# Kernel optimization log

Measured on AMD Instinct MI355X. Metric: run time of the kernel, lower is better.

The kernel has to match this reference:

```python
import jax, jax.numpy as jnp
import numpy as np

VIS_DIM = 4096
HIDDEN_D = 4096
EMB_DIM = 512
B = 128
N_NEG = 2048


def setup_inputs() -> dict:
    key = jax.random.key(0)
    k = jax.random.split(key, 7)
    vfs = jax.random.normal(k[0], (B, VIS_DIM), dtype=jnp.float32)
    p_lfs = jax.random.normal(k[1], (B, EMB_DIM), dtype=jnp.float32)
    n_lfs = jax.random.normal(k[2], (N_NEG, EMB_DIM), dtype=jnp.float32)
    # Linear params (PyTorch layout: W [out, in], y = x @ W.T + b)
    s_h = 1.0 / np.sqrt(VIS_DIM)
    s_e = 1.0 / np.sqrt(HIDDEN_D)
    W_h = jax.random.uniform(k[3], (HIDDEN_D, VIS_DIM), jnp.float32, -s_h, s_h)
    b_h = jax.random.uniform(k[4], (HIDDEN_D,), jnp.float32, -s_h, s_h)
    W_e = jax.random.uniform(k[5], (EMB_DIM, HIDDEN_D), jnp.float32, -s_e, s_e)
    b_e = jax.random.uniform(k[6], (EMB_DIM,), jnp.float32, -s_e, s_e)
    return {"vfs": vfs, "p_lfs": p_lfs, "n_lfs": n_lfs,
            "W_h": W_h, "b_h": b_h, "W_e": W_e, "b_e": b_e}


def _partial_order_sim(hypers, hypos):
    # -||relu(hypers - hypos)||_2 reduced over the last axis
    act = jax.nn.relu(hypers - hypos)
    return -jnp.sqrt(jnp.sum(act * act, axis=-1))


def reference(vfs, p_lfs, n_lfs, W_h, b_h, W_e, b_e):
    # Two plain Linears (NO ReLU in between, matching the original forward)
    vf_hidden = vfs @ W_h.T + b_h            # [B, 4096]
    vf_emb = vf_hidden @ W_e.T + b_e          # [B, emb]
    # positive score per sample
    p_scores = _partial_order_sim(p_lfs, vf_emb)                    # [B]
    # negative scores, batched over all samples at once (replaces per-sample loop)
    n_scores = _partial_order_sim(n_lfs[None, :, :], vf_emb[:, None, :])  # [B, N]
    score_stack = jnp.concatenate([p_scores[:, None], n_scores], axis=1)  # [B, N+1]
    return score_stack
```

## Files before the change

### kernel.cpp

```cpp
#include <hip/hip_runtime.h>

#define B_N  128
#define VIS  4096
#define HID  4096
#define EMB  512
#define NNEG 2048
#define OUTN (NNEG + 1)

using f32x4  = __attribute__((ext_vector_type(4))) float;
using bf16x8 = __attribute__((ext_vector_type(8))) short;

static __device__ __forceinline__ unsigned short f2bf(float f) {
  unsigned u = __builtin_bit_cast(unsigned, f);
  u += 0x7fffu + ((u >> 16) & 1u);
  return (unsigned short)(u >> 16);
}

union U16x8 { unsigned short us[8]; uint4 v; };
union U16x4 { unsigned short us[4]; uint2 v; };

static __device__ __forceinline__ void glds16(const void* g, void* l) {
  __builtin_amdgcn_global_load_lds(
      (const __attribute__((address_space(1))) unsigned*)g,
      (__attribute__((address_space(3))) unsigned*)l, 16, 0, 0);
}

__global__ __launch_bounds__(256) void prep_kernel(
    const float* __restrict__ src, unsigned short* __restrict__ dst,
    float* __restrict__ emb) {
  const int idx = blockIdx.x * 256 + threadIdx.x;
  float4 a = ((const float4*)src)[idx * 2];
  float4 b = ((const float4*)src)[idx * 2 + 1];
  U16x8 pk;
  pk.us[0] = f2bf(a.x); pk.us[1] = f2bf(a.y); pk.us[2] = f2bf(a.z); pk.us[3] = f2bf(a.w);
  pk.us[4] = f2bf(b.x); pk.us[5] = f2bf(b.y); pk.us[6] = f2bf(b.z); pk.us[7] = f2bf(b.w);
  ((uint4*)dst)[idx] = pk.v;
  if (idx < (B_N * EMB / 4))
    ((float4*)emb)[idx] = make_float4(0.f, 0.f, 0.f, 0.f);
}

__global__ __launch_bounds__(512, 2) void gemm1_kernel(
    const unsigned short* __restrict__ Abf, const float* __restrict__ Wh,
    const float* __restrict__ bh, float* __restrict__ Hp) {
  const int n0    = blockIdx.x * 32;
  const int kbase = blockIdx.y * 2048;

  __shared__ __align__(16) unsigned short As[128 * 64];
  __shared__ __align__(16) unsigned short Ws[32 * 64];

  const int t = threadIdx.x, w = t >> 6, lane = t & 63;
  const int m_lane = lane & 15, kq = lane >> 4;
  f32x4 acc[2] = {};

  const int wr = t >> 4, wc = (t & 15) * 4, Gw = (t & 15) >> 1, sub = (t & 1) * 4;
  const float* Wg = Wh + (size_t)(n0 + wr) * VIS + kbase + wc;
  float4 wv = ((const float4*)Wg)[0];
  Wg += 64;

  const int rowA = lane >> 3;
  const int gA   = (lane & 7) ^ rowA;

  for (int kt = 0; kt < 32; ++kt) {
    __syncthreads();
#pragma unroll
    for (int i = 0; i < 2; ++i) {
      const int m = i * 64 + w * 8 + rowA;
      const unsigned short* src = Abf + (size_t)m * VIS + kbase + kt * 64 + gA * 8;
      glds16(src, &As[(i * 512 + w * 64) * 8]);
    }
    {
      U16x4 pk;
      pk.us[0] = f2bf(wv.x); pk.us[1] = f2bf(wv.y); pk.us[2] = f2bf(wv.z); pk.us[3] = f2bf(wv.w);
      *(uint2*)&Ws[wr * 64 + ((Gw ^ (wr & 7)) * 8) + sub] = pk.v;
    }
    if (kt < 31) {
      wv = ((const float4*)Wg)[0];
      Wg += 64;
    }
    __syncthreads();

#pragma unroll
    for (int ks = 0; ks < 2; ++ks) {
      const int Gk = ks * 4 + kq;
      const int m0 = w * 16 + m_lane;
      bf16x8 a0 = *(const bf16x8*)&As[m0 * 64 + ((Gk ^ (m0 & 7)) * 8)];
      const int nA = m_lane, nB = m_lane + 16;
      bf16x8 b0 = *(const bf16x8*)&Ws[nA * 64 + ((Gk ^ (nA & 7)) * 8)];
      bf16x8 b1 = *(const bf16x8*)&Ws[nB * 64 + ((Gk ^ (nB & 7)) * 8)];
      acc[0] = __builtin_amdgcn_mfma_f32_16x16x32_bf16(a0, b0, acc[0], 0, 0, 0);
      acc[1] = __builtin_amdgcn_mfma_f32_16x16x32_bf16(a0, b1, acc[1], 0, 0, 0);
    }
  }

  float* Pd = Hp + (size_t)blockIdx.y * (B_N * HID);
  const int rq = (lane >> 4) * 4;
#pragma unroll
  for (int ni = 0; ni < 2; ++ni) {
    const int ng = n0 + ni * 16 + m_lane;
    const float bias = (blockIdx.y == 0) ? bh[ng] : 0.0f;
#pragma unroll
    for (int r = 0; r < 4; ++r) {
      const int mg = w * 16 + rq + r;
      Pd[(size_t)mg * HID + ng] = acc[ni][r] + bias;
    }
  }
}

__global__ __launch_bounds__(256) void cvt2_kernel(
    const float* __restrict__ Hp, unsigned short* __restrict__ dst) {
  const int idx = blockIdx.x * 256 + threadIdx.x;
  const float* H1 = Hp + (size_t)B_N * HID;
  float4 a0 = ((const float4*)Hp)[idx * 2];
  float4 b0 = ((const float4*)Hp)[idx * 2 + 1];
  float4 a1 = ((const float4*)H1)[idx * 2];
  float4 b1 = ((const float4*)H1)[idx * 2 + 1];
  U16x8 pk;
  pk.us[0] = f2bf(a0.x + a1.x); pk.us[1] = f2bf(a0.y + a1.y);
  pk.us[2] = f2bf(a0.z + a1.z); pk.us[3] = f2bf(a0.w + a1.w);
  pk.us[4] = f2bf(b0.x + b1.x); pk.us[5] = f2bf(b0.y + b1.y);
  pk.us[6] = f2bf(b0.z + b1.z); pk.us[7] = f2bf(b0.w + b1.w);
  ((uint4*)dst)[idx] = pk.v;
}

__global__ __launch_bounds__(256, 2) void gemm2_kernel(
    const unsigned short* __restrict__ Hbf, const float* __restrict__ We,
    const float* __restrict__ be, float* __restrict__ emb) {
  const int n0    = blockIdx.x * 16;
  const int kbase = blockIdx.y * 512;

  __shared__ __align__(16) unsigned short As[128 * 64];
  __shared__ __align__(16) unsigned short Ws[16 * 64];

  const int t = threadIdx.x, w = t >> 6, lane = t & 63;
  const int m_lane = lane & 15, kq = lane >> 4;
  f32x4 acc[2] = {};

  const int wr = t >> 4, wc = (t & 15) * 4;
  const float* Wg = We + (size_t)(n0 + wr) * HID + kbase + wc;
  float4 wv = ((const float4*)Wg)[0];
  Wg += 64;

  const int rowA = lane >> 3;
  const int gA   = (lane & 7) ^ rowA;

  for (int kt = 0; kt < 8; ++kt) {
    __syncthreads();
#pragma unroll
    for (int i = 0; i < 4; ++i) {
      const int m = i * 32 + w * 8 + rowA;
      const unsigned short* src = Hbf + (size_t)m * HID + kbase + kt * 64 + gA * 8;
      glds16(src, &As[(i * 256 + w * 64) * 8]);
    }
    {
      U16x4 pk;
      pk.us[0] = f2bf(wv.x); pk.us[1] = f2bf(wv.y); pk.us[2] = f2bf(wv.z); pk.us[3] = f2bf(wv.w);
      const int G = (t & 15) >> 1;
      *(uint2*)&Ws[wr * 64 + ((G ^ (wr & 7)) * 8) + (t & 1) * 4] = pk.v;
    }
    if (kt < 7) { wv = ((const float4*)Wg)[0]; Wg += 64; }
    __syncthreads();

#pragma unroll
    for (int ks = 0; ks < 2; ++ks) {
      const int Gk = ks * 4 + kq;
      const int m0 = w * 32 + m_lane, m1 = m0 + 16;
      bf16x8 a0 = *(const bf16x8*)&As[m0 * 64 + ((Gk ^ (m0 & 7)) * 8)];
      bf16x8 a1 = *(const bf16x8*)&As[m1 * 64 + ((Gk ^ (m1 & 7)) * 8)];
      bf16x8 b0 = *(const bf16x8*)&Ws[m_lane * 64 + ((Gk ^ (m_lane & 7)) * 8)];
      acc[0] = __builtin_amdgcn_mfma_f32_16x16x32_bf16(a0, b0, acc[0], 0, 0, 0);
      acc[1] = __builtin_amdgcn_mfma_f32_16x16x32_bf16(a1, b0, acc[1], 0, 0, 0);
    }
  }

  const int rq = (lane >> 4) * 4;
  const int ng = n0 + m_lane;
  const float bias = (blockIdx.y == 0) ? be[ng] : 0.0f;
#pragma unroll
  for (int mi = 0; mi < 2; ++mi) {
#pragma unroll
    for (int r = 0; r < 4; ++r) {
      const int mg = w * 32 + mi * 16 + rq + r;
      atomicAdd(&emb[mg * EMB + ng], acc[mi][r] + bias);
    }
  }
}

__global__ __launch_bounds__(256, 2) void score_kernel(
    const float* __restrict__ emb, const float* __restrict__ n_lfs,
    const float* __restrict__ p_lfs, float* __restrict__ out) {
  const int bx = blockIdx.x;
  const int t = threadIdx.x;
  const int s = t & 15, tb = t >> 4;

  if (bx < 1024) {
    const int nc = bx >> 3, bt = bx & 7;
    const int n0 = nc * 16, b0 = bt * 16;
    __shared__ __align__(16) float nl[16 * 576];
#pragma unroll
    for (int i = 0; i < 8; ++i) {
      const int f = t + i * 256;
      const int r = f >> 7, o4 = f & 127;
      float4 v = *(const float4*)(n_lfs + (size_t)(n0 + r) * EMB + o4 * 4);
      *(float4*)&nl[r * 576 + (o4 >> 3) * 36 + (o4 & 7) * 4] = v;
    }
    const float* eb = emb + (size_t)(b0 + tb) * EMB + s * 32;
    float4 ev[8];
#pragma unroll
    for (int i = 0; i < 8; ++i) ev[i] = *(const float4*)(eb + i * 4);
    __syncthreads();

    for (int j = 0; j < 16; ++j) {
      const float* nr = &nl[j * 576 + s * 36];
      float a0 = 0.f, a1 = 0.f, a2 = 0.f, a3 = 0.f;
#pragma unroll
      for (int i = 0; i < 8; ++i) {
        float4 nv = *(const float4*)(nr + i * 4);
        float d0 = fmaxf(nv.x - ev[i].x, 0.f);
        float d1 = fmaxf(nv.y - ev[i].y, 0.f);
        float d2 = fmaxf(nv.z - ev[i].z, 0.f);
        float d3 = fmaxf(nv.w - ev[i].w, 0.f);
        a0 = fmaf(d0, d0, a0); a1 = fmaf(d1, d1, a1);
        a2 = fmaf(d2, d2, a2); a3 = fmaf(d3, d3, a3);
      }
      float ss = (a0 + a1) + (a2 + a3);
      ss += __shfl_xor(ss, 1);
      ss += __shfl_xor(ss, 2);
      ss += __shfl_xor(ss, 4);
      ss += __shfl_xor(ss, 8);
      if (s == 0) out[(size_t)(b0 + tb) * OUTN + 1 + n0 + j] = -sqrtf(ss);
    }
  } else {
    const int b = (bx - 1024) * 16 + tb;
    const float* eb = emb + (size_t)b * EMB + s * 32;
    const float* pb = p_lfs + (size_t)b * EMB + s * 32;
    float a0 = 0.f, a1 = 0.f, a2 = 0.f, a3 = 0.f;
#pragma unroll
    for (int i = 0; i < 8; ++i) {
      float4 pv = *(const float4*)(pb + i * 4);
      float4 ev = *(const float4*)(eb + i * 4);
      float d0 = fmaxf(pv.x - ev.x, 0.f);
      float d1 = fmaxf(pv.y - ev.y, 0.f);
      float d2 = fmaxf(pv.z - ev.z, 0.f);
      float d3 = fmaxf(pv.w - ev.w, 0.f);
      a0 = fmaf(d0, d0, a0); a1 = fmaf(d1, d1, a1);
      a2 = fmaf(d2, d2, a2); a3 = fmaf(d3, d3, a3);
    }
    float ss = (a0 + a1) + (a2 + a3);
    ss += __shfl_xor(ss, 1);
    ss += __shfl_xor(ss, 2);
    ss += __shfl_xor(ss, 4);
    ss += __shfl_xor(ss, 8);
    if (s == 0) out[(size_t)b * OUTN] = -sqrtf(ss);
  }
}

extern "C" void kernel_launch(void* const* d_in, const int* in_sizes, int n_in,
                              void* d_out, int out_size, void* d_ws, size_t ws_size,
                              hipStream_t stream) {
  const float* vfs   = (const float*)d_in[0];
  const float* p_lfs = (const float*)d_in[1];
  const float* n_lfs = (const float*)d_in[2];
  const float* W_h   = (const float*)d_in[3];
  const float* b_h   = (const float*)d_in[4];
  const float* W_e   = (const float*)d_in[5];
  const float* b_e   = (const float*)d_in[6];
  float* out = (float*)d_out;

  char* ws = (char*)d_ws;
  float*          Hp  = (float*)ws;
  float*          emb = (float*)(ws + (4u << 20));
  unsigned short* Abf = (unsigned short*)(ws + (4u << 20) + (256u << 10));
  unsigned short* Hbf = (unsigned short*)(ws + (5u << 20) + (256u << 10));

  prep_kernel<<<256, 256, 0, stream>>>(vfs, Abf, emb);
  gemm1_kernel<<<dim3(HID / 32, 2), 512, 0, stream>>>(Abf, W_h, b_h, Hp);
  cvt2_kernel<<<256, 256, 0, stream>>>(Hp, Hbf);
  gemm2_kernel<<<dim3(EMB / 16, 8), 256, 0, stream>>>(Hbf, W_e, b_e, emb);
  score_kernel<<<1032, 256, 0, stream>>>(emb, n_lfs, p_lfs, out);
}
```

Baseline: 170.7 us.

## Load A fragments directly to registers and double-buffer W in LDS for both GEMMs

Both GEMM kernels stop staging the activation tile in LDS. Each wave now loads its A fragments straight from global memory into registers through a three-deep prefetch ring, while the converted weight tile is double-buffered in LDS so only one barrier is needed per k-step. GEMM1 splits K four ways instead of two, which doubles the grid and the partial-sum workspace, and the reduce/convert kernel now sums four partials. GEMM2 uses 512 threads with one 16x16 tile per wave, which adds register pressure and more global traffic for A in exchange for fewer LDS round-trips and syncs.

```diff
diff --git a/kernel.cpp b/kernel.cpp
--- a/kernel.cpp
+++ b/kernel.cpp
@@ -18,12 +18,9 @@
 
 union U16x8 { unsigned short us[8]; uint4 v; };
 union U16x4 { unsigned short us[4]; uint2 v; };
-
-static __device__ __forceinline__ void glds16(const void* g, void* l) {
-  __builtin_amdgcn_global_load_lds(
-      (const __attribute__((address_space(1))) unsigned*)g,
-      (__attribute__((address_space(3))) unsigned*)l, 16, 0, 0);
-}
+union U16x2 { unsigned short us[2]; unsigned v; };
+
+#define PIPE_BARRIER() __asm__ volatile("s_waitcnt lgkmcnt(0)\n\ts_barrier" ::: "memory")
 
 __global__ __launch_bounds__(256) void prep_kernel(
     const float* __restrict__ src, unsigned short* __restrict__ dst,
@@ -39,57 +36,68 @@
     ((float4*)emb)[idx] = make_float4(0.f, 0.f, 0.f, 0.f);
 }
 
-__global__ __launch_bounds__(512, 2) void gemm1_kernel(
+__global__ __launch_bounds__(512, 4) void gemm1_kernel(
     const unsigned short* __restrict__ Abf, const float* __restrict__ Wh,
     const float* __restrict__ bh, float* __restrict__ Hp) {
   const int n0    = blockIdx.x * 32;
-  const int kbase = blockIdx.y * 2048;
-
-  __shared__ __align__(16) unsigned short As[128 * 64];
-  __shared__ __align__(16) unsigned short Ws[32 * 64];
+  const int kbase = blockIdx.y * 1024;
+
+  __shared__ __align__(16) unsigned short Ws[2][32 * 64];
 
   const int t = threadIdx.x, w = t >> 6, lane = t & 63;
   const int m_lane = lane & 15, kq = lane >> 4;
   f32x4 acc[2] = {};
 
-  const int wr = t >> 4, wc = (t & 15) * 4, Gw = (t & 15) >> 1, sub = (t & 1) * 4;
-  const float* Wg = Wh + (size_t)(n0 + wr) * VIS + kbase + wc;
-  float4 wv = ((const float4*)Wg)[0];
-  Wg += 64;
-
-  const int rowA = lane >> 3;
-  const int gA   = (lane & 7) ^ rowA;
-
-  for (int kt = 0; kt < 32; ++kt) {
-    __syncthreads();
-#pragma unroll
-    for (int i = 0; i < 2; ++i) {
-      const int m = i * 64 + w * 8 + rowA;
-      const unsigned short* src = Abf + (size_t)m * VIS + kbase + kt * 64 + gA * 8;
-      glds16(src, &As[(i * 512 + w * 64) * 8]);
-    }
-    {
+  const int wr = t >> 4, Gw = (t & 15) >> 1, sub = (t & 1) * 4;
+  const float* Wg = Wh + (size_t)(n0 + wr) * VIS + kbase + (t & 15) * 4;
+  const int wofs = wr * 64 + ((Gw ^ (wr & 7)) * 8) + sub;
+
+  const int arow = w * 16 + m_lane;
+  const unsigned short* Ag = Abf + (size_t)arow * VIS + kbase + kq * 8;
+
+  float4 wv[3];
+  bf16x8 av[3][2];
+
+  wv[0] = *(const float4*)(Wg);
+  wv[1] = *(const float4*)(Wg + 64);
+  wv[2] = *(const float4*)(Wg + 128);
+  av[0][0] = *(const bf16x8*)(Ag);
+  av[0][1] = *(const bf16x8*)(Ag + 32);
+  av[1][0] = *(const bf16x8*)(Ag + 64);
+  av[1][1] = *(const bf16x8*)(Ag + 96);
+  {
+    U16x4 pk;
+    pk.us[0] = f2bf(wv[0].x); pk.us[1] = f2bf(wv[0].y);
+    pk.us[2] = f2bf(wv[0].z); pk.us[3] = f2bf(wv[0].w);
+    *(uint2*)&Ws[0][wofs] = pk.v;
+  }
+  PIPE_BARRIER();
+
+#pragma unroll
+  for (int k = 0; k < 16; ++k) {
+    const int cur = k & 1;
+    if (k + 3 < 16) wv[k % 3] = *(const float4*)(Wg + (k + 3) * 64);
+    if (k + 2 < 16) {
+      av[(k + 2) % 3][0] = *(const bf16x8*)(Ag + (k + 2) * 64);
+      av[(k + 2) % 3][1] = *(const bf16x8*)(Ag + (k + 2) * 64 + 32);
+    }
+    if (k + 1 < 16) {
+      const float4 wc = wv[(k + 1) % 3];
       U16x4 pk;
-      pk.us[0] = f2bf(wv.x); pk.us[1] = f2bf(wv.y); pk.us[2] = f2bf(wv.z); pk.us[3] = f2bf(wv.w);
-      *(uint2*)&Ws[wr * 64 + ((Gw ^ (wr & 7)) * 8) + sub] = pk.v;
-    }
-    if (kt < 31) {
-      wv = ((const float4*)Wg)[0];
-      Wg += 64;
-    }
-    __syncthreads();
-
+      pk.us[0] = f2bf(wc.x); pk.us[1] = f2bf(wc.y);
+      pk.us[2] = f2bf(wc.z); pk.us[3] = f2bf(wc.w);
+      *(uint2*)&Ws[1 - cur][wofs] = pk.v;
+    }
 #pragma unroll
     for (int ks = 0; ks < 2; ++ks) {
       const int Gk = ks * 4 + kq;
-      const int m0 = w * 16 + m_lane;
-      bf16x8 a0 = *(const bf16x8*)&As[m0 * 64 + ((Gk ^ (m0 & 7)) * 8)];
-      const int nA = m_lane, nB = m_lane + 16;
-      bf16x8 b0 = *(const bf16x8*)&Ws[nA * 64 + ((Gk ^ (nA & 7)) * 8)];
-      bf16x8 b1 = *(const bf16x8*)&Ws[nB * 64 + ((Gk ^ (nB & 7)) * 8)];
-      acc[0] = __builtin_amdgcn_mfma_f32_16x16x32_bf16(a0, b0, acc[0], 0, 0, 0);
-      acc[1] = __builtin_amdgcn_mfma_f32_16x16x32_bf16(a0, b1, acc[1], 0, 0, 0);
-    }
+      const int cA = m_lane, cB = m_lane + 16;
+      bf16x8 b0 = *(const bf16x8*)&Ws[cur][cA * 64 + ((Gk ^ (cA & 7)) * 8)];
+      bf16x8 b1 = *(const bf16x8*)&Ws[cur][cB * 64 + ((Gk ^ (cB & 7)) * 8)];
+      acc[0] = __builtin_amdgcn_mfma_f32_16x16x32_bf16(av[k % 3][ks], b0, acc[0], 0, 0, 0);
+      acc[1] = __builtin_amdgcn_mfma_f32_16x16x32_bf16(av[k % 3][ks], b1, acc[1], 0, 0, 0);
+    }
+    PIPE_BARRIER();
   }
 
   float* Pd = Hp + (size_t)blockIdx.y * (B_N * HID);
@@ -99,90 +107,95 @@
     const int ng = n0 + ni * 16 + m_lane;
     const float bias = (blockIdx.y == 0) ? bh[ng] : 0.0f;
 #pragma unroll
-    for (int r = 0; r < 4; ++r) {
-      const int mg = w * 16 + rq + r;
-      Pd[(size_t)mg * HID + ng] = acc[ni][r] + bias;
-    }
-  }
-}
-
-__global__ __launch_bounds__(256) void cvt2_kernel(
+    for (int r = 0; r < 4; ++r)
+      Pd[(size_t)(w * 16 + rq + r) * HID + ng] = acc[ni][r] + bias;
+  }
+}
+
+__global__ __launch_bounds__(256) void cvt_kernel(
     const float* __restrict__ Hp, unsigned short* __restrict__ dst) {
   const int idx = blockIdx.x * 256 + threadIdx.x;
-  const float* H1 = Hp + (size_t)B_N * HID;
-  float4 a0 = ((const float4*)Hp)[idx * 2];
-  float4 b0 = ((const float4*)Hp)[idx * 2 + 1];
-  float4 a1 = ((const float4*)H1)[idx * 2];
-  float4 b1 = ((const float4*)H1)[idx * 2 + 1];
+  const size_t PS = (size_t)B_N * HID;
+  float4 a = ((const float4*)Hp)[idx * 2];
+  float4 b = ((const float4*)Hp)[idx * 2 + 1];
+#pragma unroll
+  for (int p = 1; p < 4; ++p) {
+    float4 ap = ((const float4*)(Hp + p * PS))[idx * 2];
+    float4 bp = ((const float4*)(Hp + p * PS))[idx * 2 + 1];
+    a.x += ap.x; a.y += ap.y; a.z += ap.z; a.w += ap.w;
+    b.x += bp.x; b.y += bp.y; b.z += bp.z; b.w += bp.w;
+  }
   U16x8 pk;
-  pk.us[0] = f2bf(a0.x + a1.x); pk.us[1] = f2bf(a0.y + a1.y);
-  pk.us[2] = f2bf(a0.z + a1.z); pk.us[3] = f2bf(a0.w + a1.w);
-  pk.us[4] = f2bf(b0.x + b1.x); pk.us[5] = f2bf(b0.y + b1.y);
-  pk.us[6] = f2bf(b0.z + b1.z); pk.us[7] = f2bf(b0.w + b1.w);
+  pk.us[0] = f2bf(a.x); pk.us[1] = f2bf(a.y); pk.us[2] = f2bf(a.z); pk.us[3] = f2bf(a.w);
+  pk.us[4] = f2bf(b.x); pk.us[5] = f2bf(b.y); pk.us[6] = f2bf(b.z); pk.us[7] = f2bf(b.w);
   ((uint4*)dst)[idx] = pk.v;
 }
 
-__global__ __launch_bounds__(256, 2) void gemm2_kernel(
+__global__ __launch_bounds__(512, 4) void gemm2_kernel(
     const unsigned short* __restrict__ Hbf, const float* __restrict__ We,
     const float* __restrict__ be, float* __restrict__ emb) {
   const int n0    = blockIdx.x * 16;
   const int kbase = blockIdx.y * 512;
 
-  __shared__ __align__(16) unsigned short As[128 * 64];
-  __shared__ __align__(16) unsigned short Ws[16 * 64];
+  __shared__ __align__(16) unsigned short Ws[2][16 * 64];
 
   const int t = threadIdx.x, w = t >> 6, lane = t & 63;
   const int m_lane = lane & 15, kq = lane >> 4;
-  f32x4 acc[2] = {};
-
-  const int wr = t >> 4, wc = (t & 15) * 4;
-  const float* Wg = We + (size_t)(n0 + wr) * HID + kbase + wc;
-  float4 wv = ((const float4*)Wg)[0];
-  Wg += 64;
-
-  const int rowA = lane >> 3;
-  const int gA   = (lane & 7) ^ rowA;
-
-  for (int kt = 0; kt < 8; ++kt) {
-    __syncthreads();
-#pragma unroll
-    for (int i = 0; i < 4; ++i) {
-      const int m = i * 32 + w * 8 + rowA;
-      const unsigned short* src = Hbf + (size_t)m * HID + kbase + kt * 64 + gA * 8;
-      glds16(src, &As[(i * 256 + w * 64) * 8]);
-    }
-    {
-      U16x4 pk;
-      pk.us[0] = f2bf(wv.x); pk.us[1] = f2bf(wv.y); pk.us[2] = f2bf(wv.z); pk.us[3] = f2bf(wv.w);
-      const int G = (t & 15) >> 1;
-      *(uint2*)&Ws[wr * 64 + ((G ^ (wr & 7)) * 8) + (t & 1) * 4] = pk.v;
-    }
-    if (kt < 7) { wv = ((const float4*)Wg)[0]; Wg += 64; }
-    __syncthreads();
-
+  f32x4 acc = {};
+
+  const int wr = t >> 5, e = (t & 31) * 2;
+  const float* Wg = We + (size_t)(n0 + wr) * HID + kbase + e;
+  const int wofs = wr * 64 + (((e >> 3) ^ (wr & 7)) * 8) + (e & 7);
+
+  const int arow = w * 16 + m_lane;
+  const unsigned short* Ag = Hbf + (size_t)arow * HID + kbase + kq * 8;
+
+  float2 wv[3];
+  bf16x8 av[3][2];
+
+  wv[0] = *(const float2*)(Wg);
+  wv[1] = *(const float2*)(Wg + 64);
+  wv[2] = *(const float2*)(Wg + 128);
+  av[0][0] = *(const bf16x8*)(Ag);
+  av[0][1] = *(const bf16x8*)(Ag + 32);
+  av[1][0] = *(const bf16x8*)(Ag + 64);
+  av[1][1] = *(const bf16x8*)(Ag + 96);
+  {
+    U16x2 pk;
+    pk.us[0] = f2bf(wv[0].x); pk.us[1] = f2bf(wv[0].y);
+    *(unsigned*)&Ws[0][wofs] = pk.v;
+  }
+  PIPE_BARRIER();
+
+#pragma unroll
+  for (int k = 0; k < 8; ++k) {
+    const int cur = k & 1;
+    if (k + 3 < 8) wv[k % 3] = *(const float2*)(Wg + (k + 3) * 64);
+    if (k + 2 < 8) {
+      av[(k + 2) % 3][0] = *(const bf16x8*)(Ag + (k + 2) * 64);
+      av[(k + 2) % 3][1] = *(const bf16x8*)(Ag + (k + 2) * 64 + 32);
+    }
+    if (k + 1 < 8) {
+      const float2 wc = wv[(k + 1) % 3];
+      U16x2 pk;
+      pk.us[0] = f2bf(wc.x); pk.us[1] = f2bf(wc.y);
+      *(unsigned*)&Ws[1 - cur][wofs] = pk.v;
+    }
 #pragma unroll
     for (int ks = 0; ks < 2; ++ks) {
       const int Gk = ks * 4 + kq;
-      const int m0 = w * 32 + m_lane, m1 = m0 + 16;
-      bf16x8 a0 = *(const bf16x8*)&As[m0 * 64 + ((Gk ^ (m0 & 7)) * 8)];
-      bf16x8 a1 = *(const bf16x8*)&As[m1 * 64 + ((Gk ^ (m1 & 7)) * 8)];
-      bf16x8 b0 = *(const bf16x8*)&Ws[m_lane * 64 + ((Gk ^ (m_lane & 7)) * 8)];
-      acc[0] = __builtin_amdgcn_mfma_f32_16x16x32_bf16(a0, b0, acc[0], 0, 0, 0);
-      acc[1] = __builtin_amdgcn_mfma_f32_16x16x32_bf16(a1, b0, acc[1], 0, 0, 0);
-    }
+      bf16x8 b0 = *(const bf16x8*)&Ws[cur][m_lane * 64 + ((Gk ^ (m_lane & 7)) * 8)];
+      acc = __builtin_amdgcn_mfma_f32_16x16x32_bf16(av[k % 3][ks], b0, acc, 0, 0, 0);
+    }
+    PIPE_BARRIER();
   }
 
   const int rq = (lane >> 4) * 4;
   const int ng = n0 + m_lane;
   const float bias = (blockIdx.y == 0) ? be[ng] : 0.0f;
 #pragma unroll
-  for (int mi = 0; mi < 2; ++mi) {
-#pragma unroll
-    for (int r = 0; r < 4; ++r) {
-      const int mg = w * 32 + mi * 16 + rq + r;
-      atomicAdd(&emb[mg * EMB + ng], acc[mi][r] + bias);
-    }
-  }
+  for (int r = 0; r < 4; ++r)
+    atomicAdd(&emb[(w * 16 + rq + r) * EMB + ng], acc[r] + bias);
 }
 
 __global__ __launch_bounds__(256, 2) void score_kernel(
@@ -268,13 +281,13 @@
 
   char* ws = (char*)d_ws;
   float*          Hp  = (float*)ws;
-  float*          emb = (float*)(ws + (4u << 20));
-  unsigned short* Abf = (unsigned short*)(ws + (4u << 20) + (256u << 10));
-  unsigned short* Hbf = (unsigned short*)(ws + (5u << 20) + (256u << 10));
+  float*          emb = (float*)(ws + (8u << 20));
+  unsigned short* Abf = (unsigned short*)(ws + (8u << 20) + (256u << 10));
+  unsigned short* Hbf = (unsigned short*)(ws + (9u << 20) + (256u << 10));
 
   prep_kernel<<<256, 256, 0, stream>>>(vfs, Abf, emb);
-  gemm1_kernel<<<dim3(HID / 32, 2), 512, 0, stream>>>(Abf, W_h, b_h, Hp);
-  cvt2_kernel<<<256, 256, 0, stream>>>(Hp, Hbf);
-  gemm2_kernel<<<dim3(EMB / 16, 8), 256, 0, stream>>>(Hbf, W_e, b_e, emb);
+  gemm1_kernel<<<dim3(HID / 32, 4), 512, 0, stream>>>(Abf, W_h, b_h, Hp);
+  cvt_kernel<<<256, 256, 0, stream>>>(Hp, Hbf);
+  gemm2_kernel<<<dim3(EMB / 16, 8), 512, 0, stream>>>(Hbf, W_e, b_e, emb);
   score_kernel<<<1032, 256, 0, stream>>>(emb, n_lfs, p_lfs, out);
 }
```

Result: faster. 160.1 us (-6.2%).

## Load GEMM operands directly into registers and fuse split-K reduction into gemm2

Applied to the files above, without the earlier changes.

Both GEMM kernels stop staging tiles through LDS with barriers. Each lane now loads its MFMA fragments straight from global memory into registers, converting fp32 weights to bf16 on the fly behind a two-stage register prefetch. The cvt2 kernel is removed: gemm2 reads the two fp32 split-K partials of the hidden activations, adds them and converts them inline. gemm2's grid is also retiled to 32-column by 64-row blocks. This drops one launch, the LDS traffic and the barriers, at the cost of less coalesced global loads and redundant fetches of shared operands across waves.

```diff
diff --git a/kernel.cpp b/kernel.cpp
--- a/kernel.cpp
+++ b/kernel.cpp
@@ -8,6 +8,7 @@
 #define OUTN (NNEG + 1)
 
 using f32x4  = __attribute__((ext_vector_type(4))) float;
+using f32x8  = __attribute__((ext_vector_type(8))) float;
 using bf16x8 = __attribute__((ext_vector_type(8))) short;
 
 static __device__ __forceinline__ unsigned short f2bf(float f) {
@@ -16,14 +17,14 @@
   return (unsigned short)(u >> 16);
 }
 
+static __device__ __forceinline__ bf16x8 cvt8(f32x8 v) {
+  bf16x8 r;
+#pragma unroll
+  for (int i = 0; i < 8; ++i) r[i] = (short)f2bf(v[i]);
+  return r;
+}
+
 union U16x8 { unsigned short us[8]; uint4 v; };
-union U16x4 { unsigned short us[4]; uint2 v; };
-
-static __device__ __forceinline__ void glds16(const void* g, void* l) {
-  __builtin_amdgcn_global_load_lds(
-      (const __attribute__((address_space(1))) unsigned*)g,
-      (__attribute__((address_space(3))) unsigned*)l, 16, 0, 0);
-}
 
 __global__ __launch_bounds__(256) void prep_kernel(
     const float* __restrict__ src, unsigned short* __restrict__ dst,
@@ -45,51 +46,46 @@
   const int n0    = blockIdx.x * 32;
   const int kbase = blockIdx.y * 2048;
 
-  __shared__ __align__(16) unsigned short As[128 * 64];
-  __shared__ __align__(16) unsigned short Ws[32 * 64];
-
   const int t = threadIdx.x, w = t >> 6, lane = t & 63;
   const int m_lane = lane & 15, kq = lane >> 4;
   f32x4 acc[2] = {};
 
-  const int wr = t >> 4, wc = (t & 15) * 4, Gw = (t & 15) >> 1, sub = (t & 1) * 4;
-  const float* Wg = Wh + (size_t)(n0 + wr) * VIS + kbase + wc;
-  float4 wv = ((const float4*)Wg)[0];
-  Wg += 64;
-
-  const int rowA = lane >> 3;
-  const int gA   = (lane & 7) ^ rowA;
-
-  for (int kt = 0; kt < 32; ++kt) {
-    __syncthreads();
-#pragma unroll
-    for (int i = 0; i < 2; ++i) {
-      const int m = i * 64 + w * 8 + rowA;
-      const unsigned short* src = Abf + (size_t)m * VIS + kbase + kt * 64 + gA * 8;
-      glds16(src, &As[(i * 512 + w * 64) * 8]);
-    }
-    {
-      U16x4 pk;
-      pk.us[0] = f2bf(wv.x); pk.us[1] = f2bf(wv.y); pk.us[2] = f2bf(wv.z); pk.us[3] = f2bf(wv.w);
-      *(uint2*)&Ws[wr * 64 + ((Gw ^ (wr & 7)) * 8) + sub] = pk.v;
-    }
-    if (kt < 31) {
-      wv = ((const float4*)Wg)[0];
-      Wg += 64;
-    }
-    __syncthreads();
-
+  const unsigned short* Ag = Abf + (size_t)(w * 16 + m_lane) * VIS + kbase + kq * 8;
+  const float* W0 = Wh + (size_t)(n0 + m_lane) * VIS + kbase + kq * 8;
+  const float* W1 = W0 + (size_t)16 * VIS;
+
+  bf16x8 av[2][2];
+  f32x8  wv0[2][2], wv1[2][2];
+
+#pragma unroll
+  for (int s = 0; s < 2; ++s) {
 #pragma unroll
     for (int ks = 0; ks < 2; ++ks) {
-      const int Gk = ks * 4 + kq;
-      const int m0 = w * 16 + m_lane;
-      bf16x8 a0 = *(const bf16x8*)&As[m0 * 64 + ((Gk ^ (m0 & 7)) * 8)];
-      const int nA = m_lane, nB = m_lane + 16;
-      bf16x8 b0 = *(const bf16x8*)&Ws[nA * 64 + ((Gk ^ (nA & 7)) * 8)];
-      bf16x8 b1 = *(const bf16x8*)&Ws[nB * 64 + ((Gk ^ (nB & 7)) * 8)];
-      acc[0] = __builtin_amdgcn_mfma_f32_16x16x32_bf16(a0, b0, acc[0], 0, 0, 0);
-      acc[1] = __builtin_amdgcn_mfma_f32_16x16x32_bf16(a0, b1, acc[1], 0, 0, 0);
-    }
+      av[s][ks]  = *(const bf16x8*)(Ag + s * 64 + ks * 32);
+      wv0[s][ks] = *(const f32x8*)(W0 + s * 64 + ks * 32);
+      wv1[s][ks] = *(const f32x8*)(W1 + s * 64 + ks * 32);
+    }
+  }
+
+#pragma unroll
+  for (int k = 0; k < 32; ++k) {
+    const int s = k & 1;
+    bf16x8 b0k0 = cvt8(wv0[s][0]), b1k0 = cvt8(wv1[s][0]);
+    bf16x8 b0k1 = cvt8(wv0[s][1]), b1k1 = cvt8(wv1[s][1]);
+    bf16x8 a0 = av[s][0], a1 = av[s][1];
+    if (k + 2 < 32) {
+      const int o = (k + 2) * 64;
+#pragma unroll
+      for (int ks = 0; ks < 2; ++ks) {
+        av[s][ks]  = *(const bf16x8*)(Ag + o + ks * 32);
+        wv0[s][ks] = *(const f32x8*)(W0 + o + ks * 32);
+        wv1[s][ks] = *(const f32x8*)(W1 + o + ks * 32);
+      }
+    }
+    acc[0] = __builtin_amdgcn_mfma_f32_16x16x32_bf16(a0, b0k0, acc[0], 0, 0, 0);
+    acc[1] = __builtin_amdgcn_mfma_f32_16x16x32_bf16(a0, b1k0, acc[1], 0, 0, 0);
+    acc[0] = __builtin_amdgcn_mfma_f32_16x16x32_bf16(a1, b0k1, acc[0], 0, 0, 0);
+    acc[1] = __builtin_amdgcn_mfma_f32_16x16x32_bf16(a1, b1k1, acc[1], 0, 0, 0);
   }
 
   float* Pd = Hp + (size_t)blockIdx.y * (B_N * HID);
@@ -99,89 +95,71 @@
     const int ng = n0 + ni * 16 + m_lane;
     const float bias = (blockIdx.y == 0) ? bh[ng] : 0.0f;
 #pragma unroll
-    for (int r = 0; r < 4; ++r) {
-      const int mg = w * 16 + rq + r;
-      Pd[(size_t)mg * HID + ng] = acc[ni][r] + bias;
-    }
-  }
-}
-
-__global__ __launch_bounds__(256) void cvt2_kernel(
-    const float* __restrict__ Hp, unsigned short* __restrict__ dst) {
-  const int idx = blockIdx.x * 256 + threadIdx.x;
-  const float* H1 = Hp + (size_t)B_N * HID;
-  float4 a0 = ((const float4*)Hp)[idx * 2];
-  float4 b0 = ((const float4*)Hp)[idx * 2 + 1];
-  float4 a1 = ((const float4*)H1)[idx * 2];
-  float4 b1 = ((const float4*)H1)[idx * 2 + 1];
-  U16x8 pk;
-  pk.us[0] = f2bf(a0.x + a1.x); pk.us[1] = f2bf(a0.y + a1.y);
-  pk.us[2] = f2bf(a0.z + a1.z); pk.us[3] = f2bf(a0.w + a1.w);
-  pk.us[4] = f2bf(b0.x + b1.x); pk.us[5] = f2bf(b0.y + b1.y);
-  pk.us[6] = f2bf(b0.z + b1.z); pk.us[7] = f2bf(b0.w + b1.w);
-  ((uint4*)dst)[idx] = pk.v;
+    for (int r = 0; r < 4; ++r)
+      Pd[(size_t)(w * 16 + rq + r) * HID + ng] = acc[ni][r] + bias;
+  }
 }
 
 __global__ __launch_bounds__(256, 2) void gemm2_kernel(
-    const unsigned short* __restrict__ Hbf, const float* __restrict__ We,
+    const float* __restrict__ Hp, const float* __restrict__ We,
     const float* __restrict__ be, float* __restrict__ emb) {
-  const int n0    = blockIdx.x * 16;
+  const int n0    = blockIdx.x * 32;
   const int kbase = blockIdx.y * 512;
-
-  __shared__ __align__(16) unsigned short As[128 * 64];
-  __shared__ __align__(16) unsigned short Ws[16 * 64];
+  const int m0    = blockIdx.z * 64;
 
   const int t = threadIdx.x, w = t >> 6, lane = t & 63;
   const int m_lane = lane & 15, kq = lane >> 4;
   f32x4 acc[2] = {};
 
-  const int wr = t >> 4, wc = (t & 15) * 4;
-  const float* Wg = We + (size_t)(n0 + wr) * HID + kbase + wc;
-  float4 wv = ((const float4*)Wg)[0];
-  Wg += 64;
-
-  const int rowA = lane >> 3;
-  const int gA   = (lane & 7) ^ rowA;
-
-  for (int kt = 0; kt < 8; ++kt) {
-    __syncthreads();
-#pragma unroll
-    for (int i = 0; i < 4; ++i) {
-      const int m = i * 32 + w * 8 + rowA;
-      const unsigned short* src = Hbf + (size_t)m * HID + kbase + kt * 64 + gA * 8;
-      glds16(src, &As[(i * 256 + w * 64) * 8]);
-    }
-    {
-      U16x4 pk;
-      pk.us[0] = f2bf(wv.x); pk.us[1] = f2bf(wv.y); pk.us[2] = f2bf(wv.z); pk.us[3] = f2bf(wv.w);
-      const int G = (t & 15) >> 1;
-      *(uint2*)&Ws[wr * 64 + ((G ^ (wr & 7)) * 8) + (t & 1) * 4] = pk.v;
-    }
-    if (kt < 7) { wv = ((const float4*)Wg)[0]; Wg += 64; }
-    __syncthreads();
-
+  const float* A0 = Hp + (size_t)(m0 + w * 16 + m_lane) * HID + kbase + kq * 8;
+  const float* A1 = A0 + (size_t)B_N * HID;
+  const float* W0 = We + (size_t)(n0 + m_lane) * HID + kbase + kq * 8;
+  const float* W1 = W0 + (size_t)16 * HID;
+
+  f32x8 ap0[2][2], ap1[2][2], wv0[2][2], wv1[2][2];
+
+#pragma unroll
+  for (int s = 0; s < 2; ++s) {
 #pragma unroll
     for (int ks = 0; ks < 2; ++ks) {
-      const int Gk = ks * 4 + kq;
-      const int m0 = w * 32 + m_lane, m1 = m0 + 16;
-      bf16x8 a0 = *(const bf16x8*)&As[m0 * 64 + ((Gk ^ (m0 & 7)) * 8)];
-      bf16x8 a1 = *(const bf16x8*)&As[m1 * 64 + ((Gk ^ (m1 & 7)) * 8)];
-      bf16x8 b0 = *(const bf16x8*)&Ws[m_lane * 64 + ((Gk ^ (m_lane & 7)) * 8)];
-      acc[0] = __builtin_amdgcn_mfma_f32_16x16x32_bf16(a0, b0, acc[0], 0, 0, 0);
-      acc[1] = __builtin_amdgcn_mfma_f32_16x16x32_bf16(a1, b0, acc[1], 0, 0, 0);
-    }
+      ap0[s][ks] = *(const f32x8*)(A0 + s * 64 + ks * 32);
+      ap1[s][ks] = *(const f32x8*)(A1 + s * 64 + ks * 32);
+      wv0[s][ks] = *(const f32x8*)(W0 + s * 64 + ks * 32);
+      wv1[s][ks] = *(const f32x8*)(W1 + s * 64 + ks * 32);
+    }
+  }
+
+#pragma unroll
+  for (int k = 0; k < 8; ++k) {
+    const int s = k & 1;
+    bf16x8 a0 = cvt8(ap0[s][0] + ap1[s][0]);
+    bf16x8 a1 = cvt8(ap0[s][1] + ap1[s][1]);
+    bf16x8 b0k0 = cvt8(wv0[s][0]), b1k0 = cvt8(wv1[s][0]);
+    bf16x8 b0k1 = cvt8(wv0[s][1]), b1k1 = cvt8(wv1[s][1]);
+    if (k + 2 < 8) {
+      const int o = (k + 2) * 64;
+#pragma unroll
+      for (int ks = 0; ks < 2; ++ks) {
+        ap0[s][ks] = *(const f32x8*)(A0 + o + ks * 32);
+        ap1[s][ks] = *(const f32x8*)(A1 + o + ks * 32);
+        wv0[s][ks] = *(const f32x8*)(W0 + o + ks * 32);
+        wv1[s][ks] = *(const f32x8*)(W1 + o + ks * 32);
+      }
+    }
+    acc[0] = __builtin_amdgcn_mfma_f32_16x16x32_bf16(a0, b0k0, acc[0], 0, 0, 0);
+    acc[1] = __builtin_amdgcn_mfma_f32_16x16x32_bf16(a0, b1k0, acc[1], 0, 0, 0);
+    acc[0] = __builtin_amdgcn_mfma_f32_16x16x32_bf16(a1, b0k1, acc[0], 0, 0, 0);
+    acc[1] = __builtin_amdgcn_mfma_f32_16x16x32_bf16(a1, b1k1, acc[1], 0, 0, 0);
   }
 
   const int rq = (lane >> 4) * 4;
-  const int ng = n0 + m_lane;
-  const float bias = (blockIdx.y == 0) ? be[ng] : 0.0f;
-#pragma unroll
-  for (int mi = 0; mi < 2; ++mi) {
-#pragma unroll
-    for (int r = 0; r < 4; ++r) {
-      const int mg = w * 32 + mi * 16 + rq + r;
-      atomicAdd(&emb[mg * EMB + ng], acc[mi][r] + bias);
-    }
+#pragma unroll
+  for (int ni = 0; ni < 2; ++ni) {
+    const int ng = n0 + ni * 16 + m_lane;
+    const float bias = (blockIdx.y == 0 && blockIdx.z == 0) ? be[ng] : 0.0f;
+#pragma unroll
+    for (int r = 0; r < 4; ++r)
+      atomicAdd(&emb[(m0 + w * 16 + rq + r) * EMB + ng], acc[ni][r] + bias);
   }
 }
 
@@ -270,11 +248,9 @@
   float*          Hp  = (float*)ws;
   float*          emb = (float*)(ws + (4u << 20));
   unsigned short* Abf = (unsigned short*)(ws + (4u << 20) + (256u << 10));
-  unsigned short* Hbf = (unsigned short*)(ws + (5u << 20) + (256u << 10));
 
   prep_kernel<<<256, 256, 0, stream>>>(vfs, Abf, emb);
   gemm1_kernel<<<dim3(HID / 32, 2), 512, 0, stream>>>(Abf, W_h, b_h, Hp);
-  cvt2_kernel<<<256, 256, 0, stream>>>(Hp, Hbf);
-  gemm2_kernel<<<dim3(EMB / 16, 8), 256, 0, stream>>>(Hbf, W_e, b_e, emb);
+  gemm2_kernel<<<dim3(EMB / 32, 8, 2), 256, 0, stream>>>(Hp, W_e, b_e, emb);
   score_kernel<<<1032, 256, 0, stream>>>(emb, n_lfs, p_lfs, out);
 }
```

Measured after the change: 214.3 us. +25.6%, slower.
